# Optimization experiments

Hardware: AMD Instinct MI355X
Metric: run time of the kernel (lower is better)

The kernel has to match this reference:

```python
import jax, jax.numpy as jnp
import numpy as np

K = 5               # kernel size of the causal/dilated convs
N_LAYERS = 30       # params.n_dilation_conv_layers
CYCLE = 10          # n_dilation_conv_layers / n_dilation_cycles
MU = 255.0          # quantization_channels - 1 for mu-law expansion
B, T = 8, 262144


def dil_causal_conv(x, w, b, d):
    """Single-channel dilated causal conv. x:[B,1,T], w:[K], b:scalar/[1]."""
    P = (K - 1) * d
    xp = jnp.pad(x, ((0, 0), (0, 0), (P, 0)))
    Tn = x.shape[-1]
    # cross-correlation, matching torch Conv1d with left pad then right crop
    y = w[0] * xp[..., 0:Tn]
    for j in range(1, K):
        y = y + w[j] * xp[..., j * d: j * d + Tn]
    return y + b


def setup_inputs() -> dict:
    key = jax.random.key(0)
    ks = jax.random.split(key, 14)
    n = lambda k, shape, s=0.2: jax.random.normal(k, shape, dtype=jnp.float32) * s
    return {
        "x": jax.random.normal(ks[0], (B, 1, T), dtype=jnp.float32),
        "causal_w": n(ks[1], (K,)),
        "causal_b": n(ks[2], (1,)),
        "filter_w": n(ks[3], (N_LAYERS, K)),
        "filter_b": n(ks[4], (N_LAYERS,)),
        "gate_w": n(ks[5], (N_LAYERS, K)),
        "gate_b": n(ks[6], (N_LAYERS,)),
        "res_w": n(ks[7], (N_LAYERS,)),
        "res_b": n(ks[8], (N_LAYERS,)),
        "conv1_w": n(ks[9], (1,)),
        "conv1_b": n(ks[10], (1,)),
        "conv2_w": n(ks[11], (1,)),
        "conv2_b": n(ks[12], (1,)),
    }


def reference(x, causal_w, causal_b, filter_w, filter_b, gate_w, gate_b,
              res_w, res_b, conv1_w, conv1_b, conv2_w, conv2_b):
    dilations = [2 ** (k % CYCLE) for k in range(N_LAYERS)]
    h = dil_causal_conv(x, causal_w, causal_b, 1)
    skip = jnp.zeros_like(h)
    for k, d in enumerate(dilations):
        f = jnp.tanh(dil_causal_conv(h, filter_w[k], filter_b[k], d))
        g = jax.nn.sigmoid(dil_causal_conv(h, gate_w[k], gate_b[k], d))
        o = f * g                      # gated activation (skip output)
        h = res_w[k] * o + res_b[k] + h  # 1x1 residual conv + residual add
        skip = skip + o
    out = conv1_w * jax.nn.relu(skip) + conv1_b   # 1x1 conv
    out = conv2_w * jax.nn.relu(out) + conv2_b    # 1x1 conv
    # mu-law expanding, quantization_channels=256
    out = jnp.sign(out) * jnp.expm1(jnp.abs(out) * jnp.log1p(MU)) / MU
    return jax.nn.softmax(out, axis=-1)
```

## Files before the change

### kernel.cpp

```cpp
#include <hip/hip_runtime.h>

#define T_LEN 262144
#define B_SZ 8
#define CHUNK 8192
#define HALO 4096
#define NTHREADS 1024
#define NGROUPS ((CHUNK + HALO) / 4)
#define CHUNKS_PER_ROW (T_LEN / CHUNK)
#define NBLOCKS (B_SZ * CHUNKS_PER_ROW)
#define LOG2E 1.4426950408889634f
#define NEG2LOG2E (-2.8853900817779268f)
#define NEGLOG2E  (-1.4426950408889634f)

typedef float f32x2 __attribute__((ext_vector_type(2)));
typedef float f32x4 __attribute__((ext_vector_type(4)));
typedef _Float16 f16x2 __attribute__((ext_vector_type(2)));
typedef __fp16 fp16x2 __attribute__((ext_vector_type(2)));

__device__ __forceinline__ float frcp(float x)  { return __builtin_amdgcn_rcpf(x); }
__device__ __forceinline__ float fexp2(float x) { return __builtin_amdgcn_exp2f(x); }
__device__ __forceinline__ f32x2 pair(float s)  { f32x2 r = {s, s}; return r; }
__device__ __forceinline__ f32x2 lo2(f32x4 v)   { return __builtin_shufflevector(v, v, 0, 1); }
__device__ __forceinline__ f32x2 hi2(f32x4 v)   { return __builtin_shufflevector(v, v, 2, 3); }
__device__ __forceinline__ f32x4 cat4(f32x2 a, f32x2 b) {
    f32x4 r; r.x = a.x; r.y = a.y; r.z = b.x; r.w = b.y; return r;
}
__device__ __forceinline__ unsigned b32(f16x2 v) { return __builtin_bit_cast(unsigned, v); }
__device__ __forceinline__ f16x2 hbits(unsigned u) { return __builtin_bit_cast(f16x2, u); }
__device__ __forceinline__ f16x2 hsplat(float s) { _Float16 h = (_Float16)s; f16x2 r = {h, h}; return r; }
__device__ __forceinline__ f16x2 hfma(f16x2 a, f16x2 b, f16x2 c) { return __builtin_elementwise_fma(a, b, c); }
__device__ __forceinline__ f16x2 pkrtz(float x, float y) {
    fp16x2 t = __builtin_amdgcn_cvt_pkrtz(x, y);
    return __builtin_bit_cast(f16x2, t);
}
__device__ __forceinline__ f32x4 h2f4(f16x2 a, f16x2 b) {
    f32x2 lo = __builtin_convertvector(a, f32x2);
    f32x2 hi = __builtin_convertvector(b, f32x2);
    return cat4(lo, hi);
}

__device__ __forceinline__ f32x2 pkfma2(f32x2 a, f32x2 b, f32x2 c) {
    f32x2 d;
    asm("v_pk_fma_f32 %0, %1, %2, %3" : "=v"(d) : "v"(a), "v"(b), "v"(c));
    return d;
}
__device__ __forceinline__ f32x2 pkadd2(f32x2 a, f32x2 b) {
    f32x2 d;
    asm("v_pk_add_f32 %0, %1, %2" : "=v"(d) : "v"(a), "v"(b));
    return d;
}
__device__ __forceinline__ f32x2 pksub2(f32x2 a, f32x2 b) {
    f32x2 d;
    asm("v_pk_add_f32 %0, %1, %2 neg_lo:[0,1] neg_hi:[0,1]" : "=v"(d) : "v"(a), "v"(b));
    return d;
}
__device__ __forceinline__ f32x2 pkmul2(f32x2 a, f32x2 b) {
    f32x2 d;
    asm("v_pk_mul_f32 %0, %1, %2" : "=v"(d) : "v"(a), "v"(b));
    return d;
}
__device__ __forceinline__ f32x4 pfma_v(f32x4 a, f32x4 b, f32x4 c) {
    return cat4(pkfma2(lo2(a), lo2(b), lo2(c)), pkfma2(hi2(a), hi2(b), hi2(c)));
}
__device__ __forceinline__ f32x4 padd_s(f32x2 s, f32x4 b) {
    return cat4(pkadd2(s, lo2(b)), pkadd2(s, hi2(b)));
}
__device__ __forceinline__ f32x4 psub_s(f32x2 s, f32x4 b) {
    return cat4(pksub2(s, lo2(b)), pksub2(s, hi2(b)));
}
__device__ __forceinline__ f32x4 pmul_v(f32x4 a, f32x4 b) {
    return cat4(pkmul2(lo2(a), lo2(b)), pkmul2(hi2(a), hi2(b)));
}

__device__ __forceinline__ f32x4 gate4(f32x4 af, f32x4 ag, f32x2 one) {
    f32x4 E1, E2, rc;
    E1.x = fexp2(af.x); E1.y = fexp2(af.y); E1.z = fexp2(af.z); E1.w = fexp2(af.w);
    E2.x = fexp2(ag.x); E2.y = fexp2(ag.y); E2.z = fexp2(ag.z); E2.w = fexp2(ag.w);
    f32x4 d1  = padd_s(one, E1);
    f32x4 den = pfma_v(E2, d1, d1);
    f32x4 num = psub_s(one, E1);
    rc.x = frcp(den.x); rc.y = frcp(den.y); rc.z = frcp(den.z); rc.w = frcp(den.w);
    return pmul_v(num, rc);
}
__device__ __forceinline__ float mulaw(float v, float c1wv, float c1bv, float c2wv, float c2bv) {
    float a  = __builtin_fmaf(c1wv, fmaxf(v, 0.0f), c1bv);
    float b2 = __builtin_fmaf(c2wv, fmaxf(a, 0.0f), c2bv);
    float m  = fexp2(fabsf(b2) * 8.0f) - 1.0f;
    return copysignf(m * (1.0f / 255.0f), b2);
}

template <int STAGE>
__global__ __launch_bounds__(NTHREADS, 4)
void stage_kernel(const void* __restrict__ in_,
                  const float* __restrict__ cw, const float* __restrict__ cb,
                  const float* __restrict__ fw, const float* __restrict__ fb,
                  const float* __restrict__ gw, const float* __restrict__ gb,
                  const float* __restrict__ rw, const float* __restrict__ rb,
                  uint2* __restrict__ hout, uint2* __restrict__ skbuf,
                  float* __restrict__ pout,
                  const float* __restrict__ c1w, const float* __restrict__ c1b,
                  const float* __restrict__ c2w, const float* __restrict__ c2b,
                  float2* __restrict__ blockstats)
{
    __shared__ uint2 bufl[2][NGROUPS];
    __shared__ float red[NTHREADS / 64];

    const int tid = threadIdx.x;
    const int bid = blockIdx.x;
    const int row = bid / CHUNKS_PER_ROW;
    const int chunk = bid % CHUNKS_PER_ROW;
    const int rowbase = row * T_LEN;
    const int base_t = chunk * CHUNK;
    const bool first = (chunk == 0);
    const f16x2 HZ = hsplat(0.0f);

    f16x2 hA[3], hB[3];
    if (STAGE == 0) {
        const float* inb = (const float*)in_ + rowbase + base_t - HALO;
        #pragma unroll
        for (int w = 0; w < 3; ++w) {
            int G = tid + w * NTHREADS;
            if (w == 0 && first) { hA[w] = HZ; hB[w] = HZ; }
            else {
                f32x4 v = *(const f32x4*)(inb + 4 * G);
                hA[w] = pkrtz(v.x, v.y);
                hB[w] = pkrtz(v.z, v.w);
            }
            bufl[0][G] = make_uint2(b32(hA[w]), b32(hB[w]));
        }
    } else {
        const uint2* inb = (const uint2*)in_ + ((rowbase + base_t - HALO) >> 2);
        #pragma unroll
        for (int w = 0; w < 3; ++w) {
            int G = tid + w * NTHREADS;
            uint2 u = (w == 0 && first) ? make_uint2(0u, 0u) : inb[G];
            bufl[0][G] = u;
            hA[w] = hbits(u.x); hB[w] = hbits(u.y);
        }
    }
    f16x2 s1A, s1B, s2A, s2B;
    const int skb = ((rowbase + base_t) >> 2) + tid;
    if (STAGE == 0) { s1A = HZ; s1B = HZ; s2A = HZ; s2B = HZ; }
    else {
        uint2 u1 = skbuf[skb], u2 = skbuf[skb + 1024];
        s1A = hbits(u1.x); s1B = hbits(u1.y);
        s2A = hbits(u2.x); s2B = hbits(u2.y);
    }
    __syncthreads();

    const f32x2 ONE = pair(1.0f);

    if (STAGE == 0) {
        const f16x2 C0 = hsplat(cw[4]), C1 = hsplat(cw[3]), C2 = hsplat(cw[2]),
                    C3 = hsplat(cw[1]), C4 = hsplat(cw[0]), BB = hsplat(cb[0]);
        #pragma unroll
        for (int w = 0; w < 3; ++w) {
            int G = tid + w * NTHREADS;
            int gm = G - 1; if (w == 0) gm = gm < 0 ? 0 : gm;
            uint2 P = bufl[0][gm];
            unsigned uA = b32(hA[w]), uB = b32(hB[w]);
            unsigned t1A = __builtin_amdgcn_perm(uA, P.y, 0x05040302u);
            unsigned t1B = __builtin_amdgcn_perm(uB, uA, 0x05040302u);
            unsigned t3A = __builtin_amdgcn_perm(P.y, P.x, 0x05040302u);
            f16x2 aA = hfma(C0, hA[w], BB);
            f16x2 aB = hfma(C0, hB[w], BB);
            aA = hfma(C1, hbits(t1A), aA); aB = hfma(C1, hbits(t1B), aB);
            aA = hfma(C2, hbits(P.y), aA); aB = hfma(C2, hbits(uA), aB);
            aA = hfma(C3, hbits(t3A), aA); aB = hfma(C3, hbits(t1A), aB);
            aA = hfma(C4, hbits(P.x), aA); aB = hfma(C4, hbits(P.y), aB);
            if (w == 0 && first) { aA = HZ; aB = HZ; }
            hA[w] = aA; hB[w] = aB;
            bufl[1][G] = make_uint2(b32(aA), b32(aB));
        }
        __syncthreads();
    }

    #pragma unroll
    for (int k = 0; k < 10; ++k) {
        const int c = (STAGE == 0) ? ((k + 1) & 1) : (k & 1);
        const int d = 1 << k;
        const int L = STAGE * 10 + k;
        const float* fwL = fw + 5 * L;
        const float* gwL = gw + 5 * L;
        const f16x2 WF0 = hsplat(fwL[4] * NEG2LOG2E), WF1 = hsplat(fwL[3] * NEG2LOG2E),
                    WF2 = hsplat(fwL[2] * NEG2LOG2E), WF3 = hsplat(fwL[1] * NEG2LOG2E),
                    WF4 = hsplat(fwL[0] * NEG2LOG2E);
        const f16x2 WG0 = hsplat(gwL[4] * NEGLOG2E), WG1 = hsplat(gwL[3] * NEGLOG2E),
                    WG2 = hsplat(gwL[2] * NEGLOG2E), WG3 = hsplat(gwL[1] * NEGLOG2E),
                    WG4 = hsplat(gwL[0] * NEGLOG2E);
        const f16x2 FB = hsplat(fb[L] * NEG2LOG2E), GB = hsplat(gb[L] * NEGLOG2E);
        const f16x2 RW = hsplat(rw[L]), RB = hsplat(rb[L]);
        const uint2* __restrict__ bufc = bufl[c];
        uint2* __restrict__ bufd = bufl[c ^ 1];

        #pragma unroll
        for (int w = 0; w < 3; ++w) {
            const int G = tid + w * NTHREADS;
            if (w == 0 && tid < (2 << k)) continue;
            f16x2 cA = hA[w], cB = hB[w];
            f16x2 t1a, t1b, t2a, t2b, t3a, t3b, t4a, t4b;
            if (d >= 4) {
                const int DG = d >> 2;
                const uint2* bp = bufc + (G - 4 * DG);
                uint2 U4 = bp[0], U3 = bp[DG], U2 = bp[2 * DG], U1 = bp[3 * DG];
                t1a = hbits(U1.x); t1b = hbits(U1.y);
                t2a = hbits(U2.x); t2b = hbits(U2.y);
                t3a = hbits(U3.x); t3b = hbits(U3.y);
                t4a = hbits(U4.x); t4b = hbits(U4.y);
            } else if (d == 1) {
                uint2 P = bufc[G - 1];
                unsigned uA = b32(cA);
                unsigned w1A = __builtin_amdgcn_perm(uA, P.y, 0x05040302u);
                unsigned w1B = __builtin_amdgcn_perm(b32(cB), uA, 0x05040302u);
                unsigned w3A = __builtin_amdgcn_perm(P.y, P.x, 0x05040302u);
                t1a = hbits(w1A); t1b = hbits(w1B);
                t2a = hbits(P.y); t2b = cA;
                t3a = hbits(w3A); t3b = hbits(w1A);
                t4a = hbits(P.x); t4b = hbits(P.y);
            } else {
                uint2 P = bufc[G - 1], Q = bufc[G - 2];
                t1a = hbits(P.y); t1b = cA;
                t2a = hbits(P.x); t2b = hbits(P.y);
                t3a = hbits(Q.y); t3b = hbits(P.x);
                t4a = hbits(Q.x); t4b = hbits(Q.y);
            }
            f16x2 afA = hfma(WF0, cA, FB), afB = hfma(WF0, cB, FB);
            afA = hfma(WF1, t1a, afA); afB = hfma(WF1, t1b, afB);
            afA = hfma(WF2, t2a, afA); afB = hfma(WF2, t2b, afB);
            afA = hfma(WF3, t3a, afA); afB = hfma(WF3, t3b, afB);
            afA = hfma(WF4, t4a, afA); afB = hfma(WF4, t4b, afB);
            f16x2 agA = hfma(WG0, cA, GB), agB = hfma(WG0, cB, GB);
            agA = hfma(WG1, t1a, agA); agB = hfma(WG1, t1b, agB);
            agA = hfma(WG2, t2a, agA); agB = hfma(WG2, t2b, agB);
            agA = hfma(WG3, t3a, agA); agB = hfma(WG3, t3b, agB);
            agA = hfma(WG4, t4a, agA); agB = hfma(WG4, t4b, agB);
            f32x4 o = gate4(h2f4(afA, afB), h2f4(agA, agB), ONE);
            f16x2 oA = pkrtz(o.x, o.y), oB = pkrtz(o.z, o.w);
            f16x2 nA = hfma(RW, oA, cA + RB);
            f16x2 nB = hfma(RW, oB, cB + RB);
            if (w == 0 && first) { nA = HZ; nB = HZ; }
            hA[w] = nA; hB[w] = nB;
            if (k < 9) bufd[G] = make_uint2(b32(nA), b32(nB));
            if (w == 1) { s1A = s1A + oA; s1B = s1B + oB; }
            if (w == 2) { s2A = s2A + oA; s2B = s2B + oB; }
        }
        if (k < 9) __syncthreads();
    }

    if (STAGE < 2) {
        uint2* hp = hout + ((rowbase + base_t) >> 2);
        hp[tid]        = make_uint2(b32(hA[1]), b32(hB[1]));
        hp[tid + 1024] = make_uint2(b32(hA[2]), b32(hB[2]));
        skbuf[skb]        = make_uint2(b32(s1A), b32(s1B));
        skbuf[skb + 1024] = make_uint2(b32(s2A), b32(s2B));
    } else {
        const float c1wv = c1w[0], c1bv = c1b[0], c2wv = c2w[0], c2bv = c2b[0];
        f32x4 sk1 = h2f4(s1A, s1B), sk2 = h2f4(s2A, s2B);
        f32x4 p1, p2;
        p1.x = mulaw(sk1.x, c1wv, c1bv, c2wv, c2bv);
        p1.y = mulaw(sk1.y, c1wv, c1bv, c2wv, c2bv);
        p1.z = mulaw(sk1.z, c1wv, c1bv, c2wv, c2bv);
        p1.w = mulaw(sk1.w, c1wv, c1bv, c2wv, c2bv);
        p2.x = mulaw(sk2.x, c1wv, c1bv, c2wv, c2bv);
        p2.y = mulaw(sk2.y, c1wv, c1bv, c2wv, c2bv);
        p2.z = mulaw(sk2.z, c1wv, c1bv, c2wv, c2bv);
        p2.w = mulaw(sk2.w, c1wv, c1bv, c2wv, c2bv);
        *(f32x4*)(pout + rowbase + base_t + 4 * tid)        = p1;
        *(f32x4*)(pout + rowbase + base_t + 4096 + 4 * tid) = p2;

        float pmax = fmaxf(fmaxf(fmaxf(p1.x, p1.y), fmaxf(p1.z, p1.w)),
                           fmaxf(fmaxf(p2.x, p2.y), fmaxf(p2.z, p2.w)));
        #pragma unroll
        for (int off = 32; off; off >>= 1) pmax = fmaxf(pmax, __shfl_xor(pmax, off, 64));
        if ((tid & 63) == 0) red[tid >> 6] = pmax;
        __syncthreads();
        float bmax = red[0];
        #pragma unroll
        for (int i = 1; i < NTHREADS / 64; ++i) bmax = fmaxf(bmax, red[i]);
        __syncthreads();

        float ps = fexp2((p1.x - bmax) * LOG2E) + fexp2((p1.y - bmax) * LOG2E)
                 + fexp2((p1.z - bmax) * LOG2E) + fexp2((p1.w - bmax) * LOG2E)
                 + fexp2((p2.x - bmax) * LOG2E) + fexp2((p2.y - bmax) * LOG2E)
                 + fexp2((p2.z - bmax) * LOG2E) + fexp2((p2.w - bmax) * LOG2E);
        #pragma unroll
        for (int off = 32; off; off >>= 1) ps += __shfl_xor(ps, off, 64);
        if ((tid & 63) == 0) red[tid >> 6] = ps;
        __syncthreads();
        if (tid == 0) {
            float s = 0.0f;
            #pragma unroll
            for (int i = 0; i < NTHREADS / 64; ++i) s += red[i];
            blockstats[bid] = make_float2(bmax, s);
        }
    }
}

__global__ __launch_bounds__(64)
void combine_kernel(const float2* __restrict__ bs, float2* __restrict__ rs)
{
    const int row = blockIdx.x;
    const int lane = threadIdx.x;
    float bm = -3.0e38f, s = 0.0f;
    if (lane < CHUNKS_PER_ROW) {
        float2 v = bs[row * CHUNKS_PER_ROW + lane];
        bm = v.x; s = v.y;
    }
    float m = bm;
    #pragma unroll
    for (int off = 32; off; off >>= 1) m = fmaxf(m, __shfl_xor(m, off, 64));
    float cc = s * fexp2((bm - m) * LOG2E);
    #pragma unroll
    for (int off = 32; off; off >>= 1) cc += __shfl_xor(cc, off, 64);
    if (lane == 0) rs[row] = make_float2(m, 1.0f / cc);
}

__global__ __launch_bounds__(NTHREADS)
void norm_kernel(float* __restrict__ p, const float2* __restrict__ rs)
{
    const int tid = threadIdx.x, bid = blockIdx.x;
    const int row = bid / CHUNKS_PER_ROW;
    const float2 st = rs[row];
    const int base = row * T_LEN + (bid % CHUNKS_PER_ROW) * CHUNK + 4 * tid;
    #pragma unroll
    for (int part = 0; part < 2; ++part) {
        float* q = p + base + part * 4096;
        f32x4 v = *(const f32x4*)q;
        v.x = fexp2((v.x - st.x) * LOG2E) * st.y;
        v.y = fexp2((v.y - st.x) * LOG2E) * st.y;
        v.z = fexp2((v.z - st.x) * LOG2E) * st.y;
        v.w = fexp2((v.w - st.x) * LOG2E) * st.y;
        *(f32x4*)q = v;
    }
}

extern "C" void kernel_launch(void* const* d_in, const int* in_sizes, int n_in,
                              void* d_out, int out_size, void* d_ws, size_t ws_size,
                              hipStream_t stream)
{
    (void)in_sizes; (void)n_in; (void)out_size; (void)ws_size;
    const float* x   = (const float*)d_in[0];
    const float* cw  = (const float*)d_in[1];
    const float* cb  = (const float*)d_in[2];
    const float* fw  = (const float*)d_in[3];
    const float* fb  = (const float*)d_in[4];
    const float* gw  = (const float*)d_in[5];
    const float* gb  = (const float*)d_in[6];
    const float* rw  = (const float*)d_in[7];
    const float* rb  = (const float*)d_in[8];
    const float* c1w = (const float*)d_in[9];
    const float* c1b = (const float*)d_in[10];
    const float* c2w = (const float*)d_in[11];
    const float* c2b = (const float*)d_in[12];
    float* out = (float*)d_out;

    const size_t NTOT = (size_t)B_SZ * T_LEN;
    uint2*  hA = (uint2*)d_ws;
    uint2*  hB = (uint2*)((char*)d_ws + 2 * NTOT);
    uint2*  sk = (uint2*)((char*)d_ws + 4 * NTOT);
    float2* bs = (float2*)((char*)d_ws + 6 * NTOT);
    float2* rs = (float2*)((char*)d_ws + 6 * NTOT + 8192);

    stage_kernel<0><<<NBLOCKS, NTHREADS, 0, stream>>>(x,  cw, cb, fw, fb, gw, gb, rw, rb,
                                                      hA, sk, out, c1w, c1b, c2w, c2b, bs);
    stage_kernel<1><<<NBLOCKS, NTHREADS, 0, stream>>>(hA, cw, cb, fw, fb, gw, gb, rw, rb,
                                                      hB, sk, out, c1w, c1b, c2w, c2b, bs);
    stage_kernel<2><<<NBLOCKS, NTHREADS, 0, stream>>>(hB, cw, cb, fw, fb, gw, gb, rw, rb,
                                                      nullptr, sk, out, c1w, c1b, c2w, c2b, bs);
    combine_kernel<<<B_SZ, 64, 0, stream>>>(bs, rs);
    norm_kernel<<<NBLOCKS, NTHREADS, 0, stream>>>(out, rs);
}
```

Before: 77.42 us.

## Fuse all stages and softmax into one persistent kernel with inter-block halo flags

Result: slower. 255.5 us (+230.0%).

```diff
diff --git a/kernel.cpp b/kernel.cpp
--- a/kernel.cpp
+++ b/kernel.cpp
@@ -6,8 +6,8 @@
 #define HALO 4096
 #define NTHREADS 1024
 #define NGROUPS ((CHUNK + HALO) / 4)
-#define CHUNKS_PER_ROW (T_LEN / CHUNK)
-#define NBLOCKS (B_SZ * CHUNKS_PER_ROW)
+#define CPR (T_LEN / CHUNK)
+#define NBLOCKS (B_SZ * CPR)
 #define LOG2E 1.4426950408889634f
 #define NEG2LOG2E (-2.8853900817779268f)
 #define NEGLOG2E  (-1.4426950408889634f)
@@ -89,97 +89,29 @@
     return copysignf(m * (1.0f / 255.0f), b2);
 }
 
-template <int STAGE>
-__global__ __launch_bounds__(NTHREADS, 4)
-void stage_kernel(const void* __restrict__ in_,
-                  const float* __restrict__ cw, const float* __restrict__ cb,
-                  const float* __restrict__ fw, const float* __restrict__ fb,
-                  const float* __restrict__ gw, const float* __restrict__ gb,
-                  const float* __restrict__ rw, const float* __restrict__ rb,
-                  uint2* __restrict__ hout, uint2* __restrict__ skbuf,
-                  float* __restrict__ pout,
-                  const float* __restrict__ c1w, const float* __restrict__ c1b,
-                  const float* __restrict__ c2w, const float* __restrict__ c2b,
-                  float2* __restrict__ blockstats)
+__global__ __launch_bounds__(64)
+void init_flags(unsigned* flags)
 {
-    __shared__ uint2 bufl[2][NGROUPS];
-    __shared__ float red[NTHREADS / 64];
-
-    const int tid = threadIdx.x;
-    const int bid = blockIdx.x;
-    const int row = bid / CHUNKS_PER_ROW;
-    const int chunk = bid % CHUNKS_PER_ROW;
-    const int rowbase = row * T_LEN;
-    const int base_t = chunk * CHUNK;
-    const bool first = (chunk == 0);
+    for (int i = threadIdx.x; i < 2 * NBLOCKS + B_SZ; i += 64) flags[i] = 0u;
+}
+
+template <int CSTART>
+__device__ __forceinline__ void run_cycle(
+    int Lbase, int tid, bool first,
+    const float* __restrict__ fw, const float* __restrict__ gw,
+    const float* __restrict__ fb, const float* __restrict__ gb,
+    const float* __restrict__ rw, const float* __restrict__ rb,
+    f16x2 (&hA)[3], f16x2 (&hB)[3],
+    f16x2 &s1A, f16x2 &s1B, f16x2 &s2A, f16x2 &s2B,
+    uint2 (*bufl)[NGROUPS])
+{
+    const f32x2 ONE = pair(1.0f);
     const f16x2 HZ = hsplat(0.0f);
-
-    f16x2 hA[3], hB[3];
-    if (STAGE == 0) {
-        const float* inb = (const float*)in_ + rowbase + base_t - HALO;
-        #pragma unroll
-        for (int w = 0; w < 3; ++w) {
-            int G = tid + w * NTHREADS;
-            if (w == 0 && first) { hA[w] = HZ; hB[w] = HZ; }
-            else {
-                f32x4 v = *(const f32x4*)(inb + 4 * G);
-                hA[w] = pkrtz(v.x, v.y);
-                hB[w] = pkrtz(v.z, v.w);
-            }
-            bufl[0][G] = make_uint2(b32(hA[w]), b32(hB[w]));
-        }
-    } else {
-        const uint2* inb = (const uint2*)in_ + ((rowbase + base_t - HALO) >> 2);
-        #pragma unroll
-        for (int w = 0; w < 3; ++w) {
-            int G = tid + w * NTHREADS;
-            uint2 u = (w == 0 && first) ? make_uint2(0u, 0u) : inb[G];
-            bufl[0][G] = u;
-            hA[w] = hbits(u.x); hB[w] = hbits(u.y);
-        }
-    }
-    f16x2 s1A, s1B, s2A, s2B;
-    const int skb = ((rowbase + base_t) >> 2) + tid;
-    if (STAGE == 0) { s1A = HZ; s1B = HZ; s2A = HZ; s2B = HZ; }
-    else {
-        uint2 u1 = skbuf[skb], u2 = skbuf[skb + 1024];
-        s1A = hbits(u1.x); s1B = hbits(u1.y);
-        s2A = hbits(u2.x); s2B = hbits(u2.y);
-    }
-    __syncthreads();
-
-    const f32x2 ONE = pair(1.0f);
-
-    if (STAGE == 0) {
-        const f16x2 C0 = hsplat(cw[4]), C1 = hsplat(cw[3]), C2 = hsplat(cw[2]),
-                    C3 = hsplat(cw[1]), C4 = hsplat(cw[0]), BB = hsplat(cb[0]);
-        #pragma unroll
-        for (int w = 0; w < 3; ++w) {
-            int G = tid + w * NTHREADS;
-            int gm = G - 1; if (w == 0) gm = gm < 0 ? 0 : gm;
-            uint2 P = bufl[0][gm];
-            unsigned uA = b32(hA[w]), uB = b32(hB[w]);
-            unsigned t1A = __builtin_amdgcn_perm(uA, P.y, 0x05040302u);
-            unsigned t1B = __builtin_amdgcn_perm(uB, uA, 0x05040302u);
-            unsigned t3A = __builtin_amdgcn_perm(P.y, P.x, 0x05040302u);
-            f16x2 aA = hfma(C0, hA[w], BB);
-            f16x2 aB = hfma(C0, hB[w], BB);
-            aA = hfma(C1, hbits(t1A), aA); aB = hfma(C1, hbits(t1B), aB);
-            aA = hfma(C2, hbits(P.y), aA); aB = hfma(C2, hbits(uA), aB);
-            aA = hfma(C3, hbits(t3A), aA); aB = hfma(C3, hbits(t1A), aB);
-            aA = hfma(C4, hbits(P.x), aA); aB = hfma(C4, hbits(P.y), aB);
-            if (w == 0 && first) { aA = HZ; aB = HZ; }
-            hA[w] = aA; hB[w] = aB;
-            bufl[1][G] = make_uint2(b32(aA), b32(aB));
-        }
-        __syncthreads();
-    }
-
     #pragma unroll
     for (int k = 0; k < 10; ++k) {
-        const int c = (STAGE == 0) ? ((k + 1) & 1) : (k & 1);
+        const int c = (k + CSTART) & 1;
         const int d = 1 << k;
-        const int L = STAGE * 10 + k;
+        const int L = Lbase + k;
         const float* fwL = fw + 5 * L;
         const float* gwL = gw + 5 * L;
         const f16x2 WF0 = hsplat(fwL[4] * NEG2LOG2E), WF1 = hsplat(fwL[3] * NEG2LOG2E),
@@ -246,92 +178,167 @@
         }
         if (k < 9) __syncthreads();
     }
-
-    if (STAGE < 2) {
-        uint2* hp = hout + ((rowbase + base_t) >> 2);
-        hp[tid]        = make_uint2(b32(hA[1]), b32(hB[1]));
-        hp[tid + 1024] = make_uint2(b32(hA[2]), b32(hB[2]));
-        skbuf[skb]        = make_uint2(b32(s1A), b32(s1B));
-        skbuf[skb + 1024] = make_uint2(b32(s2A), b32(s2B));
-    } else {
-        const float c1wv = c1w[0], c1bv = c1b[0], c2wv = c2w[0], c2bv = c2b[0];
-        f32x4 sk1 = h2f4(s1A, s1B), sk2 = h2f4(s2A, s2B);
-        f32x4 p1, p2;
-        p1.x = mulaw(sk1.x, c1wv, c1bv, c2wv, c2bv);
-        p1.y = mulaw(sk1.y, c1wv, c1bv, c2wv, c2bv);
-        p1.z = mulaw(sk1.z, c1wv, c1bv, c2wv, c2bv);
-        p1.w = mulaw(sk1.w, c1wv, c1bv, c2wv, c2bv);
-        p2.x = mulaw(sk2.x, c1wv, c1bv, c2wv, c2bv);
-        p2.y = mulaw(sk2.y, c1wv, c1bv, c2wv, c2bv);
-        p2.z = mulaw(sk2.z, c1wv, c1bv, c2wv, c2bv);
-        p2.w = mulaw(sk2.w, c1wv, c1bv, c2wv, c2bv);
-        *(f32x4*)(pout + rowbase + base_t + 4 * tid)        = p1;
-        *(f32x4*)(pout + rowbase + base_t + 4096 + 4 * tid) = p2;
-
-        float pmax = fmaxf(fmaxf(fmaxf(p1.x, p1.y), fmaxf(p1.z, p1.w)),
-                           fmaxf(fmaxf(p2.x, p2.y), fmaxf(p2.z, p2.w)));
+}
+
+__global__ __launch_bounds__(NTHREADS, 4)
+void wavenet_fused(const float* __restrict__ x,
+                   const float* __restrict__ cw, const float* __restrict__ cb,
+                   const float* __restrict__ fw, const float* __restrict__ fb,
+                   const float* __restrict__ gw, const float* __restrict__ gb,
+                   const float* __restrict__ rw, const float* __restrict__ rb,
+                   const float* __restrict__ c1w, const float* __restrict__ c1b,
+                   const float* __restrict__ c2w, const float* __restrict__ c2b,
+                   uint2* __restrict__ halo0, uint2* __restrict__ halo1,
+                   float2* __restrict__ bs, unsigned* __restrict__ flags,
+                   float* __restrict__ out)
+{
+    __shared__ uint2 bufl[2][NGROUPS];
+    __shared__ float red[NTHREADS / 64];
+
+    const int tid = threadIdx.x;
+    const int bid = blockIdx.x;
+    const int row = bid / CPR;
+    const int ci  = bid % CPR;
+    const int rowbase = row * T_LEN;
+    const int base_t = ci * CHUNK;
+    const bool first = (ci == 0);
+    const f16x2 HZ = hsplat(0.0f);
+    unsigned* rowcnt = flags + 2 * NBLOCKS;
+
+    f16x2 hA[3], hB[3];
+    {
+        const float* inb = x + rowbase + base_t - HALO;
         #pragma unroll
-        for (int off = 32; off; off >>= 1) pmax = fmaxf(pmax, __shfl_xor(pmax, off, 64));
-        if ((tid & 63) == 0) red[tid >> 6] = pmax;
+        for (int w = 0; w < 3; ++w) {
+            int G = tid + w * NTHREADS;
+            if (w == 0 && first) { hA[w] = HZ; hB[w] = HZ; }
+            else {
+                f32x4 v = *(const f32x4*)(inb + 4 * G);
+                hA[w] = pkrtz(v.x, v.y);
+                hB[w] = pkrtz(v.z, v.w);
+            }
+            bufl[0][G] = make_uint2(b32(hA[w]), b32(hB[w]));
+        }
+    }
+    f16x2 s1A = HZ, s1B = HZ, s2A = HZ, s2B = HZ;
+    __syncthreads();
+
+    {
+        const f16x2 C0 = hsplat(cw[4]), C1 = hsplat(cw[3]), C2 = hsplat(cw[2]),
+                    C3 = hsplat(cw[1]), C4 = hsplat(cw[0]), BB = hsplat(cb[0]);
+        #pragma unroll
+        for (int w = 0; w < 3; ++w) {
+            int G = tid + w * NTHREADS;
+            int gm = G - 1; if (w == 0) gm = gm < 0 ? 0 : gm;
+            uint2 P = bufl[0][gm];
+            unsigned uA = b32(hA[w]), uB = b32(hB[w]);
+            unsigned t1A = __builtin_amdgcn_perm(uA, P.y, 0x05040302u);
+            unsigned t1B = __builtin_amdgcn_perm(uB, uA, 0x05040302u);
+            unsigned t3A = __builtin_amdgcn_perm(P.y, P.x, 0x05040302u);
+            f16x2 aA = hfma(C0, hA[w], BB);
+            f16x2 aB = hfma(C0, hB[w], BB);
+            aA = hfma(C1, hbits(t1A), aA); aB = hfma(C1, hbits(t1B), aB);
+            aA = hfma(C2, hbits(P.y), aA); aB = hfma(C2, hbits(uA), aB);
+            aA = hfma(C3, hbits(t3A), aA); aB = hfma(C3, hbits(t1A), aB);
+            aA = hfma(C4, hbits(P.x), aA); aB = hfma(C4, hbits(P.y), aB);
+            if (w == 0 && first) { aA = HZ; aB = HZ; }
+            hA[w] = aA; hB[w] = aB;
+            bufl[1][G] = make_uint2(b32(aA), b32(aB));
+        }
         __syncthreads();
-        float bmax = red[0];
+    }
+
+    run_cycle<1>(0, tid, first, fw, gw, fb, gb, rw, rb, hA, hB, s1A, s1B, s2A, s2B, bufl);
+
+    #pragma unroll
+    for (int s = 0; s < 2; ++s) {
+        uint2* halo = (s == 0) ? halo0 : halo1;
+        unsigned* flg = flags + s * NBLOCKS;
+        halo[(unsigned)bid * 1024u + tid] = make_uint2(b32(hA[2]), b32(hB[2]));
+        __threadfence();
+        __syncthreads();
+        if (tid == 0) atomicExch(&flg[bid], 1u);
+        if (!first) {
+            if (tid == 0) {
+                while (atomicAdd(&flg[bid - 1], 0u) == 0u) __builtin_amdgcn_s_sleep(1);
+                __threadfence();
+            }
+            __syncthreads();
+        }
+        uint2 u0 = first ? make_uint2(0u, 0u) : halo[(unsigned)(bid - 1) * 1024u + tid];
+        hA[0] = hbits(u0.x); hB[0] = hbits(u0.y);
+        bufl[0][tid]        = u0;
+        bufl[0][tid + 1024] = make_uint2(b32(hA[1]), b32(hB[1]));
+        bufl[0][tid + 2048] = make_uint2(b32(hA[2]), b32(hB[2]));
+        __syncthreads();
+        run_cycle<0>(10 * (s + 1), tid, first, fw, gw, fb, gb, rw, rb,
+                     hA, hB, s1A, s1B, s2A, s2B, bufl);
+    }
+
+    const float c1wv = c1w[0], c1bv = c1b[0], c2wv = c2w[0], c2bv = c2b[0];
+    f32x4 sk1 = h2f4(s1A, s1B), sk2 = h2f4(s2A, s2B);
+    f32x4 p1, p2;
+    p1.x = mulaw(sk1.x, c1wv, c1bv, c2wv, c2bv);
+    p1.y = mulaw(sk1.y, c1wv, c1bv, c2wv, c2bv);
+    p1.z = mulaw(sk1.z, c1wv, c1bv, c2wv, c2bv);
+    p1.w = mulaw(sk1.w, c1wv, c1bv, c2wv, c2bv);
+    p2.x = mulaw(sk2.x, c1wv, c1bv, c2wv, c2bv);
+    p2.y = mulaw(sk2.y, c1wv, c1bv, c2wv, c2bv);
+    p2.z = mulaw(sk2.z, c1wv, c1bv, c2wv, c2bv);
+    p2.w = mulaw(sk2.w, c1wv, c1bv, c2wv, c2bv);
+
+    float pmax = fmaxf(fmaxf(fmaxf(p1.x, p1.y), fmaxf(p1.z, p1.w)),
+                       fmaxf(fmaxf(p2.x, p2.y), fmaxf(p2.z, p2.w)));
+    #pragma unroll
+    for (int off = 32; off; off >>= 1) pmax = fmaxf(pmax, __shfl_xor(pmax, off, 64));
+    if ((tid & 63) == 0) red[tid >> 6] = pmax;
+    __syncthreads();
+    float bmax = red[0];
+    #pragma unroll
+    for (int i = 1; i < NTHREADS / 64; ++i) bmax = fmaxf(bmax, red[i]);
+    __syncthreads();
+
+    float ps = fexp2((p1.x - bmax) * LOG2E) + fexp2((p1.y - bmax) * LOG2E)
+             + fexp2((p1.z - bmax) * LOG2E) + fexp2((p1.w - bmax) * LOG2E)
+             + fexp2((p2.x - bmax) * LOG2E) + fexp2((p2.y - bmax) * LOG2E)
+             + fexp2((p2.z - bmax) * LOG2E) + fexp2((p2.w - bmax) * LOG2E);
+    #pragma unroll
+    for (int off = 32; off; off >>= 1) ps += __shfl_xor(ps, off, 64);
+    if ((tid & 63) == 0) red[tid >> 6] = ps;
+    __syncthreads();
+
+    if (tid == 0) {
+        float s = 0.0f;
         #pragma unroll
-        for (int i = 1; i < NTHREADS / 64; ++i) bmax = fmaxf(bmax, red[i]);
-        __syncthreads();
-
-        float ps = fexp2((p1.x - bmax) * LOG2E) + fexp2((p1.y - bmax) * LOG2E)
-                 + fexp2((p1.z - bmax) * LOG2E) + fexp2((p1.w - bmax) * LOG2E)
-                 + fexp2((p2.x - bmax) * LOG2E) + fexp2((p2.y - bmax) * LOG2E)
-                 + fexp2((p2.z - bmax) * LOG2E) + fexp2((p2.w - bmax) * LOG2E);
-        #pragma unroll
-        for (int off = 32; off; off >>= 1) ps += __shfl_xor(ps, off, 64);
-        if ((tid & 63) == 0) red[tid >> 6] = ps;
-        __syncthreads();
-        if (tid == 0) {
-            float s = 0.0f;
-            #pragma unroll
-            for (int i = 0; i < NTHREADS / 64; ++i) s += red[i];
-            blockstats[bid] = make_float2(bmax, s);
-        }
-    }
-}
-
-__global__ __launch_bounds__(64)
-void combine_kernel(const float2* __restrict__ bs, float2* __restrict__ rs)
-{
-    const int row = blockIdx.x;
-    const int lane = threadIdx.x;
-    float bm = -3.0e38f, s = 0.0f;
-    if (lane < CHUNKS_PER_ROW) {
-        float2 v = bs[row * CHUNKS_PER_ROW + lane];
-        bm = v.x; s = v.y;
-    }
-    float m = bm;
-    #pragma unroll
-    for (int off = 32; off; off >>= 1) m = fmaxf(m, __shfl_xor(m, off, 64));
-    float cc = s * fexp2((bm - m) * LOG2E);
-    #pragma unroll
-    for (int off = 32; off; off >>= 1) cc += __shfl_xor(cc, off, 64);
-    if (lane == 0) rs[row] = make_float2(m, 1.0f / cc);
-}
-
-__global__ __launch_bounds__(NTHREADS)
-void norm_kernel(float* __restrict__ p, const float2* __restrict__ rs)
-{
-    const int tid = threadIdx.x, bid = blockIdx.x;
-    const int row = bid / CHUNKS_PER_ROW;
-    const float2 st = rs[row];
-    const int base = row * T_LEN + (bid % CHUNKS_PER_ROW) * CHUNK + 4 * tid;
-    #pragma unroll
-    for (int part = 0; part < 2; ++part) {
-        float* q = p + base + part * 4096;
-        f32x4 v = *(const f32x4*)q;
-        v.x = fexp2((v.x - st.x) * LOG2E) * st.y;
-        v.y = fexp2((v.y - st.x) * LOG2E) * st.y;
-        v.z = fexp2((v.z - st.x) * LOG2E) * st.y;
-        v.w = fexp2((v.w - st.x) * LOG2E) * st.y;
-        *(f32x4*)q = v;
-    }
+        for (int i = 0; i < NTHREADS / 64; ++i) s += red[i];
+        bs[bid] = make_float2(bmax, s);
+        __threadfence();
+        atomicAdd(&rowcnt[row], 1u);
+        while (atomicAdd(&rowcnt[row], 0u) < (unsigned)CPR) __builtin_amdgcn_s_sleep(1);
+        __threadfence();
+    }
+    __syncthreads();
+
+    float m = -3.0e38f;
+    for (int j = 0; j < CPR; ++j) m = fmaxf(m, bs[row * CPR + j].x);
+    float cc = 0.0f;
+    for (int j = 0; j < CPR; ++j) {
+        float2 v = bs[row * CPR + j];
+        cc += v.y * fexp2((v.x - m) * LOG2E);
+    }
+    const float inv = 1.0f / cc;
+
+    f32x4 q1, q2;
+    q1.x = fexp2((p1.x - m) * LOG2E) * inv;
+    q1.y = fexp2((p1.y - m) * LOG2E) * inv;
+    q1.z = fexp2((p1.z - m) * LOG2E) * inv;
+    q1.w = fexp2((p1.w - m) * LOG2E) * inv;
+    q2.x = fexp2((p2.x - m) * LOG2E) * inv;
+    q2.y = fexp2((p2.y - m) * LOG2E) * inv;
+    q2.z = fexp2((p2.z - m) * LOG2E) * inv;
+    q2.w = fexp2((p2.w - m) * LOG2E) * inv;
+    *(f32x4*)(out + rowbase + base_t + 4 * tid)        = q1;
+    *(f32x4*)(out + rowbase + base_t + 4096 + 4 * tid) = q2;
 }
 
 extern "C" void kernel_launch(void* const* d_in, const int* in_sizes, int n_in,
@@ -354,19 +361,13 @@
     const float* c2b = (const float*)d_in[12];
     float* out = (float*)d_out;
 
-    const size_t NTOT = (size_t)B_SZ * T_LEN;
-    uint2*  hA = (uint2*)d_ws;
-    uint2*  hB = (uint2*)((char*)d_ws + 2 * NTOT);
-    uint2*  sk = (uint2*)((char*)d_ws + 4 * NTOT);
-    float2* bs = (float2*)((char*)d_ws + 6 * NTOT);
-    float2* rs = (float2*)((char*)d_ws + 6 * NTOT + 8192);
-
-    stage_kernel<0><<<NBLOCKS, NTHREADS, 0, stream>>>(x,  cw, cb, fw, fb, gw, gb, rw, rb,
-                                                      hA, sk, out, c1w, c1b, c2w, c2b, bs);
-    stage_kernel<1><<<NBLOCKS, NTHREADS, 0, stream>>>(hA, cw, cb, fw, fb, gw, gb, rw, rb,
-                                                      hB, sk, out, c1w, c1b, c2w, c2b, bs);
-    stage_kernel<2><<<NBLOCKS, NTHREADS, 0, stream>>>(hB, cw, cb, fw, fb, gw, gb, rw, rb,
-                                                      nullptr, sk, out, c1w, c1b, c2w, c2b, bs);
-    combine_kernel<<<B_SZ, 64, 0, stream>>>(bs, rs);
-    norm_kernel<<<NBLOCKS, NTHREADS, 0, stream>>>(out, rs);
-}
+    uint2*    halo0 = (uint2*)d_ws;
+    uint2*    halo1 = (uint2*)((char*)d_ws + (NBLOCKS * 1024 * 8));
+    float2*   bs    = (float2*)((char*)d_ws + 2 * (NBLOCKS * 1024 * 8));
+    unsigned* flags = (unsigned*)((char*)d_ws + 2 * (NBLOCKS * 1024 * 8) + 4096);
+
+    init_flags<<<1, 64, 0, stream>>>(flags);
+    wavenet_fused<<<NBLOCKS, NTHREADS, 0, stream>>>(x, cw, cb, fw, fb, gw, gb, rw, rb,
+                                                    c1w, c1b, c2w, c2b,
+                                                    halo0, halo1, bs, flags, out);
+}
```

## Store pre-softmax logits as fp16 and fold combine into norm kernel

Applied to the files above, without the earlier changes.

Measured after the change: 74.35 us, median of 2. 4.0% less time.

```diff
diff --git a/kernel.cpp b/kernel.cpp
--- a/kernel.cpp
+++ b/kernel.cpp
@@ -97,7 +97,7 @@
                   const float* __restrict__ gw, const float* __restrict__ gb,
                   const float* __restrict__ rw, const float* __restrict__ rb,
                   uint2* __restrict__ hout, uint2* __restrict__ skbuf,
-                  float* __restrict__ pout,
+                  uint2* __restrict__ pout,
                   const float* __restrict__ c1w, const float* __restrict__ c1b,
                   const float* __restrict__ c2w, const float* __restrict__ c2b,
                   float2* __restrict__ blockstats)
@@ -265,8 +265,12 @@
         p2.y = mulaw(sk2.y, c1wv, c1bv, c2wv, c2bv);
         p2.z = mulaw(sk2.z, c1wv, c1bv, c2wv, c2bv);
         p2.w = mulaw(sk2.w, c1wv, c1bv, c2wv, c2bv);
-        *(f32x4*)(pout + rowbase + base_t + 4 * tid)        = p1;
-        *(f32x4*)(pout + rowbase + base_t + 4096 + 4 * tid) = p2;
+        f16x2 q1A = pkrtz(p1.x, p1.y), q1B = pkrtz(p1.z, p1.w);
+        f16x2 q2A = pkrtz(p2.x, p2.y), q2B = pkrtz(p2.z, p2.w);
+        pout[skb]        = make_uint2(b32(q1A), b32(q1B));
+        pout[skb + 1024] = make_uint2(b32(q2A), b32(q2B));
+        p1 = h2f4(q1A, q1B);
+        p2 = h2f4(q2A, q2B);
 
         float pmax = fmaxf(fmaxf(fmaxf(p1.x, p1.y), fmaxf(p1.z, p1.w)),
                            fmaxf(fmaxf(p2.x, p2.y), fmaxf(p2.z, p2.w)));
@@ -296,41 +300,34 @@
     }
 }
 
-__global__ __launch_bounds__(64)
-void combine_kernel(const float2* __restrict__ bs, float2* __restrict__ rs)
-{
-    const int row = blockIdx.x;
-    const int lane = threadIdx.x;
-    float bm = -3.0e38f, s = 0.0f;
-    if (lane < CHUNKS_PER_ROW) {
-        float2 v = bs[row * CHUNKS_PER_ROW + lane];
-        bm = v.x; s = v.y;
-    }
-    float m = bm;
-    #pragma unroll
-    for (int off = 32; off; off >>= 1) m = fmaxf(m, __shfl_xor(m, off, 64));
-    float cc = s * fexp2((bm - m) * LOG2E);
-    #pragma unroll
-    for (int off = 32; off; off >>= 1) cc += __shfl_xor(cc, off, 64);
-    if (lane == 0) rs[row] = make_float2(m, 1.0f / cc);
-}
-
 __global__ __launch_bounds__(NTHREADS)
-void norm_kernel(float* __restrict__ p, const float2* __restrict__ rs)
+void norm_kernel(const uint2* __restrict__ p16, const float2* __restrict__ bs,
+                 float* __restrict__ out)
 {
     const int tid = threadIdx.x, bid = blockIdx.x;
     const int row = bid / CHUNKS_PER_ROW;
-    const float2 st = rs[row];
-    const int base = row * T_LEN + (bid % CHUNKS_PER_ROW) * CHUNK + 4 * tid;
+    float m = -3.0e38f;
+    #pragma unroll
+    for (int j = 0; j < CHUNKS_PER_ROW; ++j)
+        m = fmaxf(m, bs[row * CHUNKS_PER_ROW + j].x);
+    float cc = 0.0f;
+    #pragma unroll
+    for (int j = 0; j < CHUNKS_PER_ROW; ++j) {
+        float2 v = bs[row * CHUNKS_PER_ROW + j];
+        cc += v.y * fexp2((v.x - m) * LOG2E);
+    }
+    const float inv = 1.0f / cc;
+    const int base4 = ((row * T_LEN + (bid % CHUNKS_PER_ROW) * CHUNK) >> 2) + tid;
     #pragma unroll
     for (int part = 0; part < 2; ++part) {
-        float* q = p + base + part * 4096;
-        f32x4 v = *(const f32x4*)q;
-        v.x = fexp2((v.x - st.x) * LOG2E) * st.y;
-        v.y = fexp2((v.y - st.x) * LOG2E) * st.y;
-        v.z = fexp2((v.z - st.x) * LOG2E) * st.y;
-        v.w = fexp2((v.w - st.x) * LOG2E) * st.y;
-        *(f32x4*)q = v;
+        uint2 u = p16[base4 + part * NTHREADS];
+        f32x4 v = h2f4(hbits(u.x), hbits(u.y));
+        f32x4 q;
+        q.x = fexp2((v.x - m) * LOG2E) * inv;
+        q.y = fexp2((v.y - m) * LOG2E) * inv;
+        q.z = fexp2((v.z - m) * LOG2E) * inv;
+        q.w = fexp2((v.w - m) * LOG2E) * inv;
+        *(f32x4*)(out + 4 * (base4 + part * NTHREADS)) = q;
     }
 }
 
@@ -359,14 +356,12 @@
     uint2*  hB = (uint2*)((char*)d_ws + 2 * NTOT);
     uint2*  sk = (uint2*)((char*)d_ws + 4 * NTOT);
     float2* bs = (float2*)((char*)d_ws + 6 * NTOT);
-    float2* rs = (float2*)((char*)d_ws + 6 * NTOT + 8192);
 
     stage_kernel<0><<<NBLOCKS, NTHREADS, 0, stream>>>(x,  cw, cb, fw, fb, gw, gb, rw, rb,
-                                                      hA, sk, out, c1w, c1b, c2w, c2b, bs);
+                                                      hA, sk, nullptr, c1w, c1b, c2w, c2b, bs);
     stage_kernel<1><<<NBLOCKS, NTHREADS, 0, stream>>>(hA, cw, cb, fw, fb, gw, gb, rw, rb,
-                                                      hB, sk, out, c1w, c1b, c2w, c2b, bs);
+                                                      hB, sk, nullptr, c1w, c1b, c2w, c2b, bs);
     stage_kernel<2><<<NBLOCKS, NTHREADS, 0, stream>>>(hB, cw, cb, fw, fb, gw, gb, rw, rb,
-                                                      nullptr, sk, out, c1w, c1b, c2w, c2b, bs);
-    combine_kernel<<<B_SZ, 64, 0, stream>>>(bs, rs);
-    norm_kernel<<<NBLOCKS, NTHREADS, 0, stream>>>(out, rs);
-}
+                                                      nullptr, sk, hA, c1w, c1b, c2w, c2b, bs);
+    norm_kernel<<<NBLOCKS, NTHREADS, 0, stream>>>(hA, bs, out);
+}
```
